# Kernel optimization log

Measured on AMD Instinct MI355X. Metric: run time of the kernel, lower is better.

The kernel has to match this reference:

```python
import math
import jax, jax.numpy as jnp
import numpy as np

B, NP = 256, 3
LAT, TXT, D = 512, 768, 768
NL = 6
DI, DS, DC = 2 * D, 16, 4
DTR = math.ceil(D / 16)
EPS = 1e-5


def _silu(x):
    return x * jax.nn.sigmoid(x)


def _layernorm(x, g, b):
    m = x.mean(-1, keepdims=True)
    v = ((x - m) ** 2).mean(-1, keepdims=True)
    return (x - m) / jnp.sqrt(v + EPS) * g + b


def _mamba(x, in_w, conv_w, conv_b, xproj_w, dt_w, dt_b, Alog, Dp, out_w):
    # x: [B, L, D]; standard Mamba(d_state=16, d_conv=4, expand=2)
    Bb, L, _ = x.shape
    xz = jnp.einsum('bld,ed->ble', x, in_w)          # [B, L, 2*DI]
    u, z = jnp.split(xz, 2, axis=-1)
    # depthwise causal conv (kernel DC, left pad DC-1, truncated to L)
    up = jnp.pad(u, ((0, 0), (DC - 1, 0), (0, 0)))
    uc = conv_b + sum(conv_w[:, k] * up[:, k:k + L, :] for k in range(DC))
    uc = _silu(uc)
    xdbl = jnp.einsum('bld,ed->ble', uc, xproj_w)    # [B, L, DTR+2*DS]
    dt, Bm, Cm = jnp.split(xdbl, [DTR, DTR + DS], axis=-1)
    dt = jax.nn.softplus(jnp.einsum('blr,dr->bld', dt, dt_w) + dt_b)  # [B,L,DI]
    A = -jnp.exp(Alog)                               # [DI, DS]

    def step(h, xs):
        dt_t, B_t, C_t, u_t = xs                     # [B,DI],[B,DS],[B,DS],[B,DI]
        dA = jnp.exp(dt_t[..., None] * A)            # [B,DI,DS]
        h = h * dA + (dt_t * u_t)[..., None] * B_t[:, None, :]
        y = jnp.einsum('bds,bs->bd', h, C_t)
        return h, y

    h0 = jnp.zeros((Bb, DI, DS), x.dtype)
    xs = (dt.transpose(1, 0, 2), Bm.transpose(1, 0, 2),
          Cm.transpose(1, 0, 2), uc.transpose(1, 0, 2))
    _, ys = jax.lax.scan(step, h0, xs)
    y = ys.transpose(1, 0, 2) + Dp * uc
    y = y * _silu(z)
    return jnp.einsum('bld,ed->ble', y, out_w)       # [B, L, D]


def _forward(z_noisy, timestep, text_emb,
             zin_w, zin_b, tin_w, tin_b, time_w, time_b, part_emb,
             local_w, local_b, f_w, f_b, fuse_w, fuse_b, final_w, final_b,
             ln_g, ln_b, m_in_w, m_conv_w, m_conv_b, m_xproj_w, m_dt_w,
             m_dt_b, m_Alog, m_Dp, m_out_w, oln_g, oln_b, zout_w, zout_b):
    z_feat = jnp.einsum('bpl,dl->bpd', z_noisy, zin_w) + zin_b + part_emb
    text_feat = (text_emb @ tin_w.T + tin_b)[:, None]            # [B,1,D]
    half = D // 2
    freqs = jnp.exp(-math.log(10000.0) * jnp.arange(half, dtype=jnp.float32) / half)
    targ = timestep.astype(jnp.float32)[:, None] * freqs
    temb = jnp.concatenate([jnp.cos(targ), jnp.sin(targ)], -1)   # [B,D]
    time_feat = (temb @ time_w.T + time_b)[:, None]              # [B,1,D]
    x = jnp.concatenate([time_feat, text_feat, z_feat], 1)       # [B,5,D]
    # sinusoidal position embedding (first 5 rows of max_len=10 table)
    pos = jnp.arange(5, dtype=jnp.float32)[:, None]
    div = jnp.exp(jnp.arange(0, D, 2, dtype=jnp.float32) * (-math.log(10000.0) / D))
    pe = jnp.zeros((5, D), jnp.float32)
    pe = pe.at[:, 0::2].set(jnp.sin(pos * div)).at[:, 1::2].set(jnp.cos(pos * div))
    x = x + pe[None]
    text_cond = x[:, 1, :]                                       # [B,D]
    for i in range(NL):
        residual = x
        xl = _silu(jnp.einsum('bld,ed->ble', x, local_w[i]) + local_b[i])
        y_rep = jnp.broadcast_to(text_cond[:, None, :], xl.shape)
        yhat = jnp.einsum('bld,ed->ble', jnp.concatenate([xl, y_rep], -1), f_w[i]) + f_b[i]
        y_gate = y_rep * jax.nn.sigmoid(yhat)
        xt = jnp.einsum('bld,ed->ble', jnp.concatenate([xl, y_gate], -1), fuse_w[i]) + fuse_b[i]
        mf = lambda v, d: _mamba(v, m_in_w[i, d], m_conv_w[i, d], m_conv_b[i, d],
                                 m_xproj_w[i, d], m_dt_w[i, d], m_dt_b[i, d],
                                 m_Alog[i, d], m_Dp[i, d], m_out_w[i, d])
        xf = mf(xt, 0)
        xb = jnp.flip(mf(jnp.flip(xt, 1), 1), 1)
        xo = jnp.einsum('bld,ed->ble', jnp.concatenate([xf, xb], -1), final_w[i]) + final_b[i]
        x = _layernorm(xo + residual, ln_g[i], ln_b[i])
    z_out = x[:, 2:, :]                                          # [B,3,D]
    return jnp.einsum('bpd,ld->bpl', _layernorm(z_out, oln_g, oln_b), zout_w) + zout_b


def setup_inputs() -> dict:
    key = jax.random.key(0)
    kit = iter(jax.random.split(key, 40))

    def rn(shape, s=0.02):
        return jax.random.normal(next(kit), shape, jnp.float32) * s

    inp = dict(
        z_noisy=jax.random.normal(next(kit), (B, NP, LAT), jnp.float32),
        text_emb=jax.random.normal(next(kit), (B, TXT), jnp.float32),
        zin_w=rn((D, LAT)), zin_b=jnp.zeros((D,), jnp.float32),
        tin_w=rn((D, TXT)), tin_b=jnp.zeros((D,), jnp.float32),
        time_w=rn((D, D)), time_b=jnp.zeros((D,), jnp.float32),
        part_emb=rn((1, NP, D)),
        local_w=rn((NL, D, D)), local_b=jnp.zeros((NL, D), jnp.float32),
        f_w=rn((NL, D, 2 * D)), f_b=jnp.zeros((NL, D), jnp.float32),
        fuse_w=rn((NL, D, 2 * D)), fuse_b=jnp.zeros((NL, D), jnp.float32),
        final_w=rn((NL, D, 2 * D)), final_b=jnp.zeros((NL, D), jnp.float32),
        ln_g=jnp.ones((NL, D), jnp.float32), ln_b=jnp.zeros((NL, D), jnp.float32),
        m_in_w=rn((NL, 2, 2 * DI, D)),
        m_conv_w=rn((NL, 2, DI, DC), 0.1),
        m_conv_b=jnp.zeros((NL, 2, DI), jnp.float32),
        m_xproj_w=rn((NL, 2, DTR + 2 * DS, DI)),
        m_dt_w=rn((NL, 2, DI, DTR), 0.1),
        m_dt_b=jnp.full((NL, 2, DI), -4.6, jnp.float32),
        m_Alog=jnp.tile(jnp.log(jnp.arange(1, DS + 1, dtype=jnp.float32)), (NL, 2, DI, 1)),
        m_Dp=jnp.ones((NL, 2, DI), jnp.float32),
        m_out_w=rn((NL, 2, D, DI)),
        oln_g=jnp.ones((D,), jnp.float32), oln_b=jnp.zeros((D,), jnp.float32),
        zout_w=rn((LAT, D)), zout_b=jnp.zeros((LAT,), jnp.float32),
        timestep=jax.random.randint(next(kit), (B,), 0, 1000),
    )
    return inp


def reference(z_noisy, text_emb, zin_w, zin_b, tin_w, tin_b, time_w, time_b,
              part_emb, local_w, local_b, f_w, f_b, fuse_w, fuse_b, final_w,
              final_b, ln_g, ln_b, m_in_w, m_conv_w, m_conv_b, m_xproj_w,
              m_dt_w, m_dt_b, m_Alog, m_Dp, m_out_w, oln_g, oln_b, zout_w,
              zout_b, timestep):
    return _forward(z_noisy, timestep, text_emb, zin_w, zin_b, tin_w, tin_b,
                    time_w, time_b, part_emb, local_w, local_b, f_w, f_b,
                    fuse_w, fuse_b, final_w, final_b, ln_g, ln_b, m_in_w,
                    m_conv_w, m_conv_b, m_xproj_w, m_dt_w, m_dt_b, m_Alog,
                    m_Dp, m_out_w, oln_g, oln_b, zout_w, zout_b)
```

## Files before the change

kernel.cpp:

```cpp
#include <hip/hip_runtime.h>
#include <hip/hip_bf16.h>
#include <math.h>

#define B_   256
#define NP_  3
#define LAT_ 512
#define TXT_ 768
#define D_   768
#define NL_  6
#define DI_  1536
#define DS_  16
#define DC_  4
#define DTR_ 48
#define L_   5
#define M_   (B_*L_)
#define EPS_ 1e-5f

#define OB_WBF    0ull
#define OB_XPP    139591680ull
#define OB_TEMB   144310272ull
#define OB_ZNORM  144703488ull
#define OB_XBF    145883136ull
#define OB_TCBF   147849216ull
#define OB_CAT1   148242432ull
#define OB_XTBF   152174592ull
#define OB_XZBF   154140672ull
#define OB_UCY    169869312ull
#define OB_CAT2   177733632ull
#define OB_X      181665792ull
#define OB_TC     185597952ull
#define OB_TCF    186384384ull
#define OB_ZFEAT  187170816ull
#define OB_XO     189530112ull
#define OB_PART   193462272ull

#define WO_LOCAL  0u
#define WO_F      3538944u
#define WO_FUSE   10616832u
#define WO_FINAL  17694720u
#define WO_IN     24772608u
#define WO_OUT    53084160u
#define WO_ZIN    67239936u
#define WO_TIN    67633152u
#define WO_TIME   68222976u
#define WO_ZOUT   68812800u
#define WO_ZNOISY 69206016u
#define WO_TEXT   69599232u
#define WO_END    69795840u

typedef __attribute__((ext_vector_type(4))) float floatx4;
typedef __attribute__((ext_vector_type(8))) short short8;
typedef __attribute__((ext_vector_type(8))) unsigned short ushort8v;

__device__ __forceinline__ float sigm(float v) { return 1.f / (1.f + expf(-v)); }
__device__ __forceinline__ float softplus(float v) {
    return fmaxf(v, 0.f) + log1pf(expf(-fabsf(v)));
}
__device__ __forceinline__ unsigned short bf16rn(float f) {
    unsigned int u = __builtin_bit_cast(unsigned int, f);
    u = (u + 0x7fffu + ((u >> 16) & 1u)) >> 16;
    return (unsigned short)u;
}
__device__ __forceinline__ float b2f(unsigned short u) {
    unsigned int x = ((unsigned int)u) << 16;
    return __builtin_bit_cast(float, x);
}

template<int N> __device__ __forceinline__ void waitv() {
    asm volatile("s_waitcnt vmcnt(%0)" :: "i"(N) : "memory");
}

struct CvtArgs { const float* s[12]; };

__global__ __launch_bounds__(256) void cvt_kernel(CvtArgs a, unsigned short* __restrict__ dst)
{
    constexpr unsigned ends[12] = {
        3538944u, 10616832u, 17694720u, 24772608u, 53084160u, 67239936u,
        67633152u, 68222976u, 68812800u, 69206016u, 69599232u, 69795840u };
    unsigned i16 = (blockIdx.x * 256u + threadIdx.x) * 16u;
    if (i16 >= WO_END) return;
    int t = 0;
    while (i16 >= ends[t]) ++t;
    unsigned start = t ? ends[t - 1] : 0u;
    const float* s = a.s[t] + (i16 - start);
    floatx4 v0 = *(const floatx4*)s;
    floatx4 v1 = *(const floatx4*)(s + 4);
    floatx4 v2 = *(const floatx4*)(s + 8);
    floatx4 v3 = *(const floatx4*)(s + 12);
    ushort8v o0 = { bf16rn(v0[0]), bf16rn(v0[1]), bf16rn(v0[2]), bf16rn(v0[3]),
                    bf16rn(v1[0]), bf16rn(v1[1]), bf16rn(v1[2]), bf16rn(v1[3]) };
    ushort8v o1 = { bf16rn(v2[0]), bf16rn(v2[1]), bf16rn(v2[2]), bf16rn(v2[3]),
                    bf16rn(v3[0]), bf16rn(v3[1]), bf16rn(v3[2]), bf16rn(v3[3]) };
    *(ushort8v*)(dst + i16) = o0;
    *(ushort8v*)(dst + i16 + 8) = o1;
}

__global__ __launch_bounds__(256) void xpad_kernel(const float* __restrict__ xw,
                                                   unsigned short* __restrict__ dst)
{
    unsigned i8 = (blockIdx.x * 256u + threadIdx.x) * 8u;
    if (i8 >= 12u * 128u * 1536u) return;
    unsigned pi = i8 / (128u * 1536u);
    unsigned rem = i8 - pi * 128u * 1536u;
    unsigned row = rem / 1536u, col = rem - row * 1536u;
    ushort8v o = {0, 0, 0, 0, 0, 0, 0, 0};
    if (row < 80u) {
        const float* s = xw + ((size_t)pi * 80u + row) * 1536u + col;
        floatx4 v0 = *(const floatx4*)s;
        floatx4 v1 = *(const floatx4*)(s + 4);
        o = ushort8v{ bf16rn(v0[0]), bf16rn(v0[1]), bf16rn(v0[2]), bf16rn(v0[3]),
                      bf16rn(v1[0]), bf16rn(v1[1]), bf16rn(v1[2]), bf16rn(v1[3]) };
    }
    *(ushort8v*)(dst + i8) = o;
}

template<int BM, int BN, int CD, int DEPTH, int PF>
__global__ __launch_bounds__(256) void gemm_bf16_kernel(
    const unsigned short* __restrict__ A, int lda,
    const unsigned short* __restrict__ W, int wld,
    const float* __restrict__ bias,
    const float* __restrict__ aux0,
    const float* __restrict__ aux1,
    void* __restrict__ Cv, int ldc,
    int M, int N, int K, int epi, int ncap,
    int zsplit, unsigned long long zA, unsigned long long zW, unsigned long long zC)
{
    constexpr int GA = BM / 64;
    constexpr int GB = BN / 64;
    constexpr int LPS = GA + GB;
    constexpr int FRM = BM / 32;
    constexpr int FRN = BN / 32;
    constexpr int BMSK = DEPTH - 1;

    const int z = blockIdx.z;
    const int dirz = z / zsplit, ksz = z - dirz * zsplit;
    A += (unsigned long long)dirz * zA + (unsigned long long)ksz * (unsigned)K;
    W += (unsigned long long)dirz * zW + (unsigned long long)ksz * (unsigned)K;

    __shared__ unsigned short lds[DEPTH][(BM + BN) * 32];

    const int tid = threadIdx.x;
    const int m0 = blockIdx.y * BM, n0 = blockIdx.x * BN;
    const int w = tid >> 6, lane = tid & 63;
    const int wr = w >> 1, wc = w & 1;
    const int lrow = lane & 15;
    const int lk = (lane >> 4) << 3;

    const int rA = tid >> 2, sA = tid & 3;
    const int scA = ((sA ^ ((rA >> 1) & 3)) << 3);
    floatx4 acc[FRM][FRN] = {};

    auto stage = [&](int buf, int k0) {
        unsigned short* base = &lds[buf][0];
#pragma unroll
        for (int i = 0; i < GA; ++i) {
            int t = tid + i * 256;
            int r = t >> 2;
            const unsigned short* src = A + (size_t)(m0 + r) * lda + k0 + scA;
            __builtin_amdgcn_global_load_lds(
                (const __attribute__((address_space(1))) unsigned int*)(const void*)src,
                (__attribute__((address_space(3))) unsigned int*)(void*)(base + i * 2048 + w * 512),
                16, 0, 0);
        }
#pragma unroll
        for (int i = 0; i < GB; ++i) {
            int t = tid + i * 256;
            int r = t >> 2;
            const unsigned short* src = W + (size_t)(n0 + r) * wld + k0 + scA;
            __builtin_amdgcn_global_load_lds(
                (const __attribute__((address_space(1))) unsigned int*)(const void*)src,
                (__attribute__((address_space(3))) unsigned int*)(void*)(base + BM * 32 + i * 2048 + w * 512),
                16, 0, 0);
        }
    };

    const int nt = K >> 5;
#pragma unroll
    for (int s = 0; s < PF; ++s)
        if (s < nt) stage(s, s << 5);

    int offA[FRM], offB[FRN];
#pragma unroll
    for (int i = 0; i < FRM; ++i) {
        int row = wr * (BM / 2) + i * 16 + lrow;
        offA[i] = row * 32 + (lk ^ (((row >> 1) & 3) << 3));
    }
#pragma unroll
    for (int j = 0; j < FRN; ++j) {
        int row = wc * (BN / 2) + j * 16 + lrow;
        offB[j] = BM * 32 + row * 32 + (lk ^ (((row >> 1) & 3) << 3));
    }

    for (int t = 0; t < nt; ++t) {
        int rem = nt - 1 - t;
        if (rem >= PF) { stage((t + PF) & BMSK, (t + PF) << 5); waitv<PF * LPS>(); }
        else if (rem == 5) waitv<5 * LPS>();
        else if (rem == 4) waitv<4 * LPS>();
        else if (rem == 3) waitv<3 * LPS>();
        else if (rem == 2) waitv<2 * LPS>();
        else if (rem == 1) waitv<1 * LPS>();
        else               waitv<0>();
        __builtin_amdgcn_s_barrier();
        const unsigned short* pl = &lds[t & BMSK][0];
        short8 af[FRM], bfv[FRN];
#pragma unroll
        for (int i = 0; i < FRM; ++i) af[i] = *(const short8*)(pl + offA[i]);
#pragma unroll
        for (int j = 0; j < FRN; ++j) bfv[j] = *(const short8*)(pl + offB[j]);
#pragma unroll
        for (int i = 0; i < FRM; ++i)
#pragma unroll
            for (int j = 0; j < FRN; ++j)
                acc[i][j] = __builtin_amdgcn_mfma_f32_16x16x32_bf16(af[i], bfv[j], acc[i][j], 0, 0, 0);
    }

#pragma unroll
    for (int i = 0; i < FRM; ++i) {
        int row0 = m0 + wr * (BM / 2) + i * 16 + (lane >> 4) * 4;
#pragma unroll
        for (int j = 0; j < FRN; ++j) {
            int col = n0 + wc * (BN / 2) + j * 16 + lrow;
            if (col >= ncap) continue;
            float bb = bias ? bias[col] : 0.f;
#pragma unroll
            for (int r = 0; r < 4; ++r) {
                int row = row0 + r;
                float v = acc[i][j][r] + bb;
                if (epi == 1) {
                    v = v * sigm(v);
                } else if (epi == 3) {
                    int b = row / 5;
                    v = acc[i][j][r] + aux0[(size_t)b * 768 + col];
                    v = aux1[(size_t)b * 768 + col] * sigm(v);
                }
                size_t off = (size_t)z * zC + (size_t)row * ldc + col;
                if (CD == 1) ((float*)Cv)[off] = v;
                else         ((unsigned short*)Cv)[off] = bf16rn(v);
            }
        }
    }
}

__global__ void temb_kernel(const int* __restrict__ ts, unsigned short* __restrict__ temb)
{
    int idx = blockIdx.x * blockDim.x + threadIdx.x;
    if (idx >= B_ * 384) return;
    int j = idx % 384, b = idx / 384;
    float f = expf(-logf(10000.f) * (float)j / 384.f);
    float targ = (float)ts[b] * f;
    temb[(size_t)b * D_ + j]       = bf16rn(cosf(targ));
    temb[(size_t)b * D_ + 384 + j] = bf16rn(sinf(targ));
}

__global__ void finalize_embed_kernel(float* __restrict__ x,
                                      unsigned short* __restrict__ xbf,
                                      const float* __restrict__ zfeat,
                                      const float* __restrict__ part_emb,
                                      float* __restrict__ tc,
                                      unsigned short* __restrict__ tcbf)
{
    int idx = blockIdx.x * blockDim.x + threadIdx.x;
    if (idx >= B_ * L_ * D_) return;
    int d = idx % D_;
    int bl = idx / D_;
    int l = bl % L_, b = bl / L_;
    float v;
    if (l >= 2) v = zfeat[((size_t)(b * 3 + (l - 2))) * D_ + d] + part_emb[(size_t)(l - 2) * D_ + d];
    else        v = x[idx];
    int j = d >> 1;
    float dv = expf((float)(2 * j) * (-logf(10000.f) / (float)D_));
    float ang = (float)l * dv;
    v += (d & 1) ? cosf(ang) : sinf(ang);
    x[idx] = v;
    xbf[idx] = bf16rn(v);
    if (l == 1) { tc[(size_t)b * D_ + d] = v; tcbf[(size_t)b * D_ + d] = bf16rn(v); }
}

__global__ void conv_silu_kernel(const unsigned short* __restrict__ xz,
                                 const float* __restrict__ cw,
                                 const float* __restrict__ cb,
                                 unsigned short* __restrict__ ucy)
{
    int idx = blockIdx.x * blockDim.x + threadIdx.x;
    if (idx >= 2 * M_ * DI_) return;
    int ch = idx % DI_;
    int t2 = idx / DI_;
    int bl = t2 % M_, dir = t2 / M_;
    int l = bl % L_, b = bl / L_;
    float v = cb[dir * DI_ + ch];
    const float* wp = cw + ((size_t)(dir * DI_ + ch)) * DC_;
#pragma unroll
    for (int k = 0; k < DC_; ++k) {
        int lp = dir ? (l + 3 - k) : (l + k - 3);
        if (lp >= 0 && lp < L_)
            v += wp[k] * b2f(xz[((size_t)(b * L_ + lp)) * 6144 + dir * 3072 + ch]);
    }
    ucy[idx] = bf16rn(v * sigm(v));
}

__global__ __launch_bounds__(256) void dtscan_kernel(
    const float* __restrict__ part,
    unsigned short* ucy,
    const unsigned short* __restrict__ xz,
    const float* __restrict__ dt_w,
    const float* __restrict__ dt_b,
    const float* __restrict__ Alog,
    const float* __restrict__ Dp)
{
    __shared__ float xd[L_][80];
    const int dir = blockIdx.z;
    const int b = blockIdx.y;
    const int ch = blockIdx.x * 256 + threadIdx.x;

    for (int o = threadIdx.x; o < L_ * 80; o += 256) {
        int l = o / 80, n = o - l * 80;
        float s = 0.f;
#pragma unroll
        for (int ks = 0; ks < 8; ++ks)
            s += part[((size_t)(dir * 8 + ks) * M_ + b * L_ + l) * 80 + n];
        xd[l][n] = s;
    }
    __syncthreads();

    const int cg = dir * DI_ + ch;
    float dt[L_];
    const float* wp = dt_w + (size_t)cg * DTR_;
    float dbv = dt_b[cg];
#pragma unroll
    for (int l = 0; l < L_; ++l) {
        float v = dbv;
#pragma unroll
        for (int r = 0; r < DTR_; ++r) v = fmaf(xd[l][r], wp[r], v);
        dt[l] = softplus(v);
    }

    float Aa[DS_], h[DS_];
#pragma unroll
    for (int s = 0; s < DS_; ++s) { Aa[s] = -expf(Alog[(size_t)cg * DS_ + s]); h[s] = 0.f; }
    float Dv = Dp[cg];

#pragma unroll
    for (int t = 0; t < L_; ++t) {
        const int l = dir ? (L_ - 1 - t) : t;
        size_t base = (size_t)(b * L_ + l);
        size_t uoff = ((size_t)dir * M_ + base) * DI_ + ch;
        float dtv = dt[l];
        float ucv = b2f(ucy[uoff]);
        float du = dtv * ucv;
        float y = 0.f;
#pragma unroll
        for (int s = 0; s < DS_; ++s) {
            h[s] = h[s] * expf(dtv * Aa[s]) + du * xd[l][48 + s];
            y = fmaf(h[s], xd[l][64 + s], y);
        }
        float zv = b2f(xz[base * 6144 + dir * 3072 + 1536 + ch]);
        ucy[uoff] = bf16rn((y + Dv * ucv) * (zv * sigm(zv)));
    }
}

__device__ __forceinline__ float block_sum(float v)
{
    __shared__ float sd[4];
#pragma unroll
    for (int o = 1; o < 64; o <<= 1) v += __shfl_xor(v, o, 64);
    int lane = threadIdx.x & 63, wid = threadIdx.x >> 6;
    if (lane == 0) sd[wid] = v;
    __syncthreads();
    v = sd[0] + sd[1] + sd[2] + sd[3];
    __syncthreads();
    return v;
}

__global__ __launch_bounds__(256) void ln_residual_kernel(
    const float* __restrict__ xo, float* __restrict__ x,
    unsigned short* __restrict__ xbf,
    const float* __restrict__ g, const float* __restrict__ bt)
{
    int row = blockIdx.x;
    const float* pa = xo + (size_t)row * D_;
    float* px = x + (size_t)row * D_;
    float v[3];
    float s = 0.f;
#pragma unroll
    for (int i = 0; i < 3; ++i) { int d = threadIdx.x + 256 * i; v[i] = pa[d] + px[d]; s += v[i]; }
    float mean = block_sum(s) * (1.f / (float)D_);
    float sq = 0.f;
#pragma unroll
    for (int i = 0; i < 3; ++i) { float t = v[i] - mean; sq += t * t; }
    float var = block_sum(sq) * (1.f / (float)D_);
    float inv = rsqrtf(var + EPS_);
#pragma unroll
    for (int i = 0; i < 3; ++i) {
        int d = threadIdx.x + 256 * i;
        float o = (v[i] - mean) * inv * g[d] + bt[d];
        px[d] = o;
        xbf[(size_t)row * D_ + d] = bf16rn(o);
    }
}

__global__ __launch_bounds__(256) void ln_out_kernel(
    const float* __restrict__ x, const float* __restrict__ g,
    const float* __restrict__ bt, unsigned short* __restrict__ znorm)
{
    int row = blockIdx.x;
    int b = row / 3, p = row % 3;
    const float* pa = x + ((size_t)(b * L_ + 2 + p)) * D_;
    float v[3];
    float s = 0.f;
#pragma unroll
    for (int i = 0; i < 3; ++i) { int d = threadIdx.x + 256 * i; v[i] = pa[d]; s += v[i]; }
    float mean = block_sum(s) * (1.f / (float)D_);
    float sq = 0.f;
#pragma unroll
    for (int i = 0; i < 3; ++i) { float t = v[i] - mean; sq += t * t; }
    float var = block_sum(sq) * (1.f / (float)D_);
    float inv = rsqrtf(var + EPS_);
#pragma unroll
    for (int i = 0; i < 3; ++i) {
        int d = threadIdx.x + 256 * i;
        znorm[(size_t)row * D_ + d] = bf16rn((v[i] - mean) * inv * g[d] + bt[d]);
    }
}

extern "C" void kernel_launch(void* const* d_in, const int* in_sizes, int n_in,
                              void* d_out, int out_size, void* d_ws, size_t ws_size,
                              hipStream_t stream)
{
    const float* z_noisy  = (const float*)d_in[0];
    const float* text_emb = (const float*)d_in[1];
    const float* zin_b    = (const float*)d_in[3];
    const float* tin_b    = (const float*)d_in[5];
    const float* time_b   = (const float*)d_in[7];
    const float* part_emb = (const float*)d_in[8];
    const float* local_b  = (const float*)d_in[10];
    const float* f_b      = (const float*)d_in[12];
    const float* fuse_b   = (const float*)d_in[14];
    const float* final_b  = (const float*)d_in[16];
    const float* ln_g     = (const float*)d_in[17];
    const float* ln_b     = (const float*)d_in[18];
    const float* m_conv_w = (const float*)d_in[20];
    const float* m_conv_b = (const float*)d_in[21];
    const float* m_xproj_w= (const float*)d_in[22];
    const float* m_dt_w   = (const float*)d_in[23];
    const float* m_dt_b   = (const float*)d_in[24];
    const float* m_Alog   = (const float*)d_in[25];
    const float* m_Dp     = (const float*)d_in[26];
    const float* oln_g    = (const float*)d_in[28];
    const float* oln_b    = (const float*)d_in[29];
    const float* zout_b   = (const float*)d_in[31];
    const int*   timestep = (const int*)d_in[32];

    char* wsb = (char*)d_ws;
    unsigned short* wbf   = (unsigned short*)(wsb + OB_WBF);
    unsigned short* xpp   = (unsigned short*)(wsb + OB_XPP);
    unsigned short* tembb = (unsigned short*)(wsb + OB_TEMB);
    unsigned short* znormb= (unsigned short*)(wsb + OB_ZNORM);
    unsigned short* xbf   = (unsigned short*)(wsb + OB_XBF);
    unsigned short* tcbf  = (unsigned short*)(wsb + OB_TCBF);
    unsigned short* cat1b = (unsigned short*)(wsb + OB_CAT1);
    unsigned short* xtbf  = (unsigned short*)(wsb + OB_XTBF);
    unsigned short* xzbf  = (unsigned short*)(wsb + OB_XZBF);
    unsigned short* ucy   = (unsigned short*)(wsb + OB_UCY);
    unsigned short* cat2b = (unsigned short*)(wsb + OB_CAT2);
    float* x     = (float*)(wsb + OB_X);
    float* tc    = (float*)(wsb + OB_TC);
    float* tcf   = (float*)(wsb + OB_TCF);
    float* zfeat = (float*)(wsb + OB_ZFEAT);
    float* xo    = (float*)(wsb + OB_XO);
    float* part  = (float*)(wsb + OB_PART);

    unsigned short* local_bf = wbf + WO_LOCAL;
    unsigned short* f_bf     = wbf + WO_F;
    unsigned short* fuse_bf  = wbf + WO_FUSE;
    unsigned short* final_bf = wbf + WO_FINAL;
    unsigned short* in_bf    = wbf + WO_IN;
    unsigned short* out_bf   = wbf + WO_OUT;
    unsigned short* zin_bf   = wbf + WO_ZIN;
    unsigned short* tin_bf   = wbf + WO_TIN;
    unsigned short* time_bf  = wbf + WO_TIME;
    unsigned short* zout_bf  = wbf + WO_ZOUT;
    unsigned short* znz_bf   = wbf + WO_ZNOISY;
    unsigned short* text_bf  = wbf + WO_TEXT;

    auto ew = [&](int n) { return dim3((n + 255) / 256); };

    CvtArgs ca;
    ca.s[0] = (const float*)d_in[9];
    ca.s[1] = (const float*)d_in[11];
    ca.s[2] = (const float*)d_in[13];
    ca.s[3] = (const float*)d_in[15];
    ca.s[4] = (const float*)d_in[19];
    ca.s[5] = (const float*)d_in[27];
    ca.s[6] = (const float*)d_in[2];
    ca.s[7] = (const float*)d_in[4];
    ca.s[8] = (const float*)d_in[6];
    ca.s[9] = (const float*)d_in[30];
    ca.s[10] = z_noisy;
    ca.s[11] = text_emb;
    hipLaunchKernelGGL(cvt_kernel, dim3(WO_END / 16 / 256), dim3(256), 0, stream, ca, wbf);
    hipLaunchKernelGGL(xpad_kernel, dim3(12 * 128 * 1536 / 8 / 256), dim3(256), 0, stream,
                       m_xproj_w, xpp);
    hipLaunchKernelGGL(temb_kernel, ew(B_ * 384), dim3(256), 0, stream, timestep, tembb);

    auto g64d = [&](const unsigned short* A, int lda, const unsigned short* W, int wld,
                    const float* bias, const float* a0, const float* a1,
                    void* C, int ldc, int Mm, int Nn, int Kk, int epi, int ncap, int cd,
                    int gz, int zsplit, unsigned long long zA, unsigned long long zW,
                    unsigned long long zC) {
        dim3 g(Nn / 64, Mm / 64, gz);
        if (cd == 1)
            gemm_bf16_kernel<64, 64, 1, 8, 6><<<g, dim3(256), 0, stream>>>(
                A, lda, W, wld, bias, a0, a1, C, ldc, Mm, Nn, Kk, epi, ncap, zsplit, zA, zW, zC);
        else
            gemm_bf16_kernel<64, 64, 0, 8, 6><<<g, dim3(256), 0, stream>>>(
                A, lda, W, wld, bias, a0, a1, C, ldc, Mm, Nn, Kk, epi, ncap, zsplit, zA, zW, zC);
    };
    auto g64s = [&](const unsigned short* A, int lda, const unsigned short* W, int wld,
                    const float* bias, const float* a0, const float* a1,
                    void* C, int ldc, int Mm, int Nn, int Kk, int epi, int ncap, int cd,
                    int gz, int zsplit, unsigned long long zA, unsigned long long zW,
                    unsigned long long zC) {
        dim3 g(Nn / 64, Mm / 64, gz);
        if (cd == 1)
            gemm_bf16_kernel<64, 64, 1, 4, 2><<<g, dim3(256), 0, stream>>>(
                A, lda, W, wld, bias, a0, a1, C, ldc, Mm, Nn, Kk, epi, ncap, zsplit, zA, zW, zC);
        else
            gemm_bf16_kernel<64, 64, 0, 4, 2><<<g, dim3(256), 0, stream>>>(
                A, lda, W, wld, bias, a0, a1, C, ldc, Mm, Nn, Kk, epi, ncap, zsplit, zA, zW, zC);
    };

    g64d(tembb, D_, time_bf, D_, time_b, nullptr, nullptr, x, L_ * D_, B_, D_, D_, 0, D_, 1,
         1, 1, 0, 0, 0);
    g64d(text_bf, TXT_, tin_bf, TXT_, tin_b, nullptr, nullptr, x + D_, L_ * D_, B_, D_, TXT_, 0, D_, 1,
         1, 1, 0, 0, 0);
    g64d(znz_bf, LAT_, zin_bf, LAT_, zin_b, nullptr, nullptr, zfeat, D_, B_ * NP_, D_, LAT_, 0, D_, 1,
         1, 1, 0, 0, 0);
    hipLaunchKernelGGL(finalize_embed_kernel, ew(B_ * L_ * D_), dim3(256), 0, stream,
                       x, xbf, zfeat, part_emb, tc, tcbf);

    for (int i = 0; i < NL_; ++i) {
        g64d(xbf, D_, local_bf + (size_t)i * D_ * D_, D_, local_b + (size_t)i * D_,
             nullptr, nullptr, cat1b, 2 * D_, M_, D_, D_, 1, D_, 0, 1, 1, 0, 0, 0);
        g64d(tcbf, D_, f_bf + (size_t)i * D_ * 2 * D_ + D_, 2 * D_, f_b + (size_t)i * D_,
             nullptr, nullptr, tcf, D_, B_, D_, D_, 0, D_, 1, 1, 1, 0, 0, 0);
        g64d(cat1b, 2 * D_, f_bf + (size_t)i * D_ * 2 * D_, 2 * D_, nullptr,
             tcf, tc, cat1b + D_, 2 * D_, M_, D_, D_, 3, D_, 0, 1, 1, 0, 0, 0);
        g64d(cat1b, 2 * D_, fuse_bf + (size_t)i * D_ * 2 * D_, 2 * D_, fuse_b + (size_t)i * D_,
             nullptr, nullptr, xtbf, D_, M_, D_, 2 * D_, 0, D_, 0, 1, 1, 0, 0, 0);

        {
            dim3 g(6144 / 128, M_ / 64, 1);
            gemm_bf16_kernel<64, 128, 0, 4, 2><<<g, dim3(256), 0, stream>>>(
                xtbf, D_, in_bf + (size_t)i * 4718592ull, D_, nullptr, nullptr, nullptr,
                xzbf, 6144, M_, 6144, D_, 0, 6144, 1, 0, 0, 0);
        }
        hipLaunchKernelGGL(conv_silu_kernel, ew(2 * M_ * DI_), dim3(256), 0, stream,
                           xzbf, m_conv_w + (size_t)i * 2 * DI_ * DC_,
                           m_conv_b + (size_t)i * 2 * DI_, ucy);
        g64s(ucy, DI_, xpp + (size_t)i * 2 * 128 * DI_, DI_, nullptr, nullptr, nullptr,
             part, 80, M_, 128, 192, 0, 80, 1,
             16, 8, (unsigned long long)M_ * DI_, (unsigned long long)128 * DI_,
             (unsigned long long)M_ * 80);
        hipLaunchKernelGGL(dtscan_kernel, dim3(DI_ / 256, B_, 2), dim3(256), 0, stream,
                           part, ucy, xzbf,
                           m_dt_w + (size_t)i * 2 * DI_ * DTR_, m_dt_b + (size_t)i * 2 * DI_,
                           m_Alog + (size_t)i * 2 * DI_ * DS_, m_Dp + (size_t)i * 2 * DI_);
        g64s(ucy, DI_, out_bf + (size_t)i * 2 * D_ * DI_, DI_, nullptr, nullptr, nullptr,
             cat2b, 2 * D_, M_, D_, DI_, 0, D_, 0,
             2, 1, (unsigned long long)M_ * DI_, (unsigned long long)D_ * DI_, 768ull);
        g64d(cat2b, 2 * D_, final_bf + (size_t)i * D_ * 2 * D_, 2 * D_, final_b + (size_t)i * D_,
             nullptr, nullptr, xo, D_, M_, D_, 2 * D_, 0, D_, 1, 1, 1, 0, 0, 0);
        hipLaunchKernelGGL(ln_residual_kernel, dim3(M_), dim3(256), 0, stream,
                           xo, x, xbf, ln_g + (size_t)i * D_, ln_b + (size_t)i * D_);
    }

    hipLaunchKernelGGL(ln_out_kernel, dim3(B_ * NP_), dim3(256), 0, stream,
                       x, oln_g, oln_b, znormb);
    g64d(znormb, D_, zout_bf, D_, zout_b, nullptr, nullptr,
         (float*)d_out, LAT_, B_ * NP_, LAT_, D_, 0, LAT_, 1, 1, 1, 0, 0, 0);
}
```

Measured before the change: 1.223 ms.

## Use 128x128 tiles for in-proj and split-K out-proj with reduction kernel

The in-projection GEMM switches from 64x128 to 128x128 tiles, halving its grid and raising reuse per block. The out-projection now runs a 128x128 tile GEMM with split-K of 2 per direction (grid z=4), writing fp32 partials into the reused xz buffer. A new vectorised kernel sums the two partials and converts to bf16 in the concat buffer. This adds a launch and fp32 partial traffic, and relies on xz being dead once the scan has run.

```diff
diff --git a/kernel.cpp b/kernel.cpp
--- a/kernel.cpp
+++ b/kernel.cpp
@@ -51,6 +51,7 @@
 typedef __attribute__((ext_vector_type(4))) float floatx4;
 typedef __attribute__((ext_vector_type(8))) short short8;
 typedef __attribute__((ext_vector_type(8))) unsigned short ushort8v;
+typedef __attribute__((ext_vector_type(4))) unsigned short ushort4v;
 
 __device__ __forceinline__ float sigm(float v) { return 1.f / (1.f + expf(-v)); }
 __device__ __forceinline__ float softplus(float v) {
@@ -239,6 +240,24 @@
             }
         }
     }
+}
+
+__global__ __launch_bounds__(256) void reduce_out_kernel(const float* __restrict__ part,
+                                                         unsigned short* __restrict__ cat2)
+{
+    int idx = blockIdx.x * 256 + threadIdx.x;
+    if (idx >= 2 * M_ * 768 / 4) return;
+    int e4 = idx * 4;
+    int dir = e4 / (M_ * 768);
+    int rem = e4 - dir * (M_ * 768);
+    int row = rem / 768, col = rem - row * 768;
+    const float* p0 = part + ((size_t)(dir * 2)     * M_ + row) * 768 + col;
+    const float* p1 = part + ((size_t)(dir * 2 + 1) * M_ + row) * 768 + col;
+    floatx4 a = *(const floatx4*)p0;
+    floatx4 b = *(const floatx4*)p1;
+    ushort4v o = { bf16rn(a[0] + b[0]), bf16rn(a[1] + b[1]),
+                   bf16rn(a[2] + b[2]), bf16rn(a[3] + b[3]) };
+    *(ushort4v*)(cat2 + (size_t)row * 1536 + dir * 768 + col) = o;
 }
 
 __global__ void temb_kernel(const int* __restrict__ ts, unsigned short* __restrict__ temb)
@@ -468,6 +487,7 @@
     float* zfeat = (float*)(wsb + OB_ZFEAT);
     float* xo    = (float*)(wsb + OB_XO);
     float* part  = (float*)(wsb + OB_PART);
+    float* partk = (float*)(wsb + OB_XZBF);
 
     unsigned short* local_bf = wbf + WO_LOCAL;
     unsigned short* f_bf     = wbf + WO_F;
@@ -549,8 +569,8 @@
              nullptr, nullptr, xtbf, D_, M_, D_, 2 * D_, 0, D_, 0, 1, 1, 0, 0, 0);
 
         {
-            dim3 g(6144 / 128, M_ / 64, 1);
-            gemm_bf16_kernel<64, 128, 0, 4, 2><<<g, dim3(256), 0, stream>>>(
+            dim3 g(6144 / 128, M_ / 128, 1);
+            gemm_bf16_kernel<128, 128, 0, 4, 2><<<g, dim3(256), 0, stream>>>(
                 xtbf, D_, in_bf + (size_t)i * 4718592ull, D_, nullptr, nullptr, nullptr,
                 xzbf, 6144, M_, 6144, D_, 0, 6144, 1, 0, 0, 0);
         }
@@ -565,9 +585,16 @@
                            part, ucy, xzbf,
                            m_dt_w + (size_t)i * 2 * DI_ * DTR_, m_dt_b + (size_t)i * 2 * DI_,
                            m_Alog + (size_t)i * 2 * DI_ * DS_, m_Dp + (size_t)i * 2 * DI_);
-        g64s(ucy, DI_, out_bf + (size_t)i * 2 * D_ * DI_, DI_, nullptr, nullptr, nullptr,
-             cat2b, 2 * D_, M_, D_, DI_, 0, D_, 0,
-             2, 1, (unsigned long long)M_ * DI_, (unsigned long long)D_ * DI_, 768ull);
+        {
+            dim3 g(768 / 128, M_ / 128, 4);
+            gemm_bf16_kernel<128, 128, 1, 4, 2><<<g, dim3(256), 0, stream>>>(
+                ucy, DI_, out_bf + (size_t)i * 2 * D_ * DI_, DI_, nullptr, nullptr, nullptr,
+                partk, 768, M_, 768, 768, 0, 768,
+                2, (unsigned long long)M_ * DI_, (unsigned long long)D_ * DI_,
+                (unsigned long long)M_ * 768);
+        }
+        hipLaunchKernelGGL(reduce_out_kernel, dim3(2 * M_ * 768 / 4 / 256), dim3(256), 0, stream,
+                           partk, cat2b);
         g64d(cat2b, 2 * D_, final_bf + (size_t)i * D_ * 2 * D_, 2 * D_, final_b + (size_t)i * D_,
              nullptr, nullptr, xo, D_, M_, D_, 2 * D_, 0, D_, 1, 1, 1, 0, 0, 0);
         hipLaunchKernelGGL(ln_residual_kernel, dim3(M_), dim3(256), 0, stream,
```

Result: slower. 1.272 ms (+4.0%).

## Batch per-layer text-condition GEMMs into one launch and widen weight conversion

Applied to the files above, without the earlier changes.

The six per-layer tc·f_w GEMMs depend only on the text condition, so they are hoisted out of the layer loop into one batched launch (grid z = 6). The results are stored in bf16, in a buffer that reuses the zfeat region. The epilogue of the fused cat GEMM now adds the bias and reads the bf16 condition term. Separately, the fp32-to-bf16 weight conversion kernel handles 32 elements per thread with nontemporal loads, halving its grid. This removes six small kernel launches and some fp32 traffic, at the cost of bf16 rounding on the intermediate and reuse of the zfeat buffer.

```diff
diff --git a/kernel.cpp b/kernel.cpp
--- a/kernel.cpp
+++ b/kernel.cpp
@@ -77,22 +77,22 @@
     constexpr unsigned ends[12] = {
         3538944u, 10616832u, 17694720u, 24772608u, 53084160u, 67239936u,
         67633152u, 68222976u, 68812800u, 69206016u, 69599232u, 69795840u };
-    unsigned i16 = (blockIdx.x * 256u + threadIdx.x) * 16u;
-    if (i16 >= WO_END) return;
+    unsigned i32 = (blockIdx.x * 256u + threadIdx.x) * 32u;
+    if (i32 >= WO_END) return;
     int t = 0;
-    while (i16 >= ends[t]) ++t;
+    while (i32 >= ends[t]) ++t;
     unsigned start = t ? ends[t - 1] : 0u;
-    const float* s = a.s[t] + (i16 - start);
-    floatx4 v0 = *(const floatx4*)s;
-    floatx4 v1 = *(const floatx4*)(s + 4);
-    floatx4 v2 = *(const floatx4*)(s + 8);
-    floatx4 v3 = *(const floatx4*)(s + 12);
-    ushort8v o0 = { bf16rn(v0[0]), bf16rn(v0[1]), bf16rn(v0[2]), bf16rn(v0[3]),
-                    bf16rn(v1[0]), bf16rn(v1[1]), bf16rn(v1[2]), bf16rn(v1[3]) };
-    ushort8v o1 = { bf16rn(v2[0]), bf16rn(v2[1]), bf16rn(v2[2]), bf16rn(v2[3]),
-                    bf16rn(v3[0]), bf16rn(v3[1]), bf16rn(v3[2]), bf16rn(v3[3]) };
-    *(ushort8v*)(dst + i16) = o0;
-    *(ushort8v*)(dst + i16 + 8) = o1;
+    const float* s = a.s[t] + (i32 - start);
+    floatx4 v[8];
+#pragma unroll
+    for (int q = 0; q < 8; ++q)
+        v[q] = __builtin_nontemporal_load((const floatx4*)(s + q * 4));
+#pragma unroll
+    for (int q = 0; q < 4; ++q) {
+        ushort8v o = { bf16rn(v[2*q][0]), bf16rn(v[2*q][1]), bf16rn(v[2*q][2]), bf16rn(v[2*q][3]),
+                       bf16rn(v[2*q+1][0]), bf16rn(v[2*q+1][1]), bf16rn(v[2*q+1][2]), bf16rn(v[2*q+1][3]) };
+        *(ushort8v*)(dst + i32 + q * 8) = o;
+    }
 }
 
 __global__ __launch_bounds__(256) void xpad_kernel(const float* __restrict__ xw,
@@ -230,7 +230,7 @@
                     v = v * sigm(v);
                 } else if (epi == 3) {
                     int b = row / 5;
-                    v = acc[i][j][r] + aux0[(size_t)b * 768 + col];
+                    v = acc[i][j][r] + bb + b2f(((const unsigned short*)aux0)[(size_t)b * 768 + col]);
                     v = aux1[(size_t)b * 768 + col] * sigm(v);
                 }
                 size_t off = (size_t)z * zC + (size_t)row * ldc + col;
@@ -464,8 +464,8 @@
     unsigned short* cat2b = (unsigned short*)(wsb + OB_CAT2);
     float* x     = (float*)(wsb + OB_X);
     float* tc    = (float*)(wsb + OB_TC);
-    float* tcf   = (float*)(wsb + OB_TCF);
     float* zfeat = (float*)(wsb + OB_ZFEAT);
+    unsigned short* tcf6 = (unsigned short*)(wsb + OB_ZFEAT);
     float* xo    = (float*)(wsb + OB_XO);
     float* part  = (float*)(wsb + OB_PART);
 
@@ -497,7 +497,7 @@
     ca.s[9] = (const float*)d_in[30];
     ca.s[10] = z_noisy;
     ca.s[11] = text_emb;
-    hipLaunchKernelGGL(cvt_kernel, dim3(WO_END / 16 / 256), dim3(256), 0, stream, ca, wbf);
+    hipLaunchKernelGGL(cvt_kernel, dim3(WO_END / 32 / 256), dim3(256), 0, stream, ca, wbf);
     hipLaunchKernelGGL(xpad_kernel, dim3(12 * 128 * 1536 / 8 / 256), dim3(256), 0, stream,
                        m_xproj_w, xpp);
     hipLaunchKernelGGL(temb_kernel, ew(B_ * 384), dim3(256), 0, stream, timestep, tembb);
@@ -538,13 +538,16 @@
     hipLaunchKernelGGL(finalize_embed_kernel, ew(B_ * L_ * D_), dim3(256), 0, stream,
                        x, xbf, zfeat, part_emb, tc, tcbf);
 
+    g64d(tcbf, D_, f_bf + D_, 2 * D_, nullptr, nullptr, nullptr,
+         tcf6, D_, B_, D_, D_, 0, D_, 0,
+         6, 1, 0ull, (unsigned long long)D_ * 2 * D_, (unsigned long long)B_ * D_);
+
     for (int i = 0; i < NL_; ++i) {
         g64d(xbf, D_, local_bf + (size_t)i * D_ * D_, D_, local_b + (size_t)i * D_,
              nullptr, nullptr, cat1b, 2 * D_, M_, D_, D_, 1, D_, 0, 1, 1, 0, 0, 0);
-        g64d(tcbf, D_, f_bf + (size_t)i * D_ * 2 * D_ + D_, 2 * D_, f_b + (size_t)i * D_,
-             nullptr, nullptr, tcf, D_, B_, D_, D_, 0, D_, 1, 1, 1, 0, 0, 0);
-        g64d(cat1b, 2 * D_, f_bf + (size_t)i * D_ * 2 * D_, 2 * D_, nullptr,
-             tcf, tc, cat1b + D_, 2 * D_, M_, D_, D_, 3, D_, 0, 1, 1, 0, 0, 0);
+        g64d(cat1b, 2 * D_, f_bf + (size_t)i * D_ * 2 * D_, 2 * D_, f_b + (size_t)i * D_,
+             (const float*)(tcf6 + (size_t)i * B_ * D_), tc,
+             cat1b + D_, 2 * D_, M_, D_, D_, 3, D_, 0, 1, 1, 0, 0, 0);
         g64d(cat1b, 2 * D_, fuse_bf + (size_t)i * D_ * 2 * D_, 2 * D_, fuse_b + (size_t)i * D_,
              nullptr, nullptr, xtbf, D_, M_, D_, 2 * D_, 0, D_, 0, 1, 1, 0, 0, 0);
 
```

New measurement: 1.238 ms. No clear change (+1.3%).
